# Kernel tuning notes

Hardware: AMD Instinct MI355X
Metric: run time of the kernel (lower is better)

The kernel has to match this reference:

```python
import jax, jax.numpy as jnp
import numpy as np
import math

D_MODEL = 512
NUM_HEADS = 8
B, L = 2, 4096
EPS_NORM = 1e-8
PLASTICITY = 1.0


def setup_inputs() -> dict:
    key = jax.random.key(0)
    ks = jax.random.split(key, 6)
    D, H = D_MODEL, NUM_HEADS
    std = 1.0 / math.sqrt(D)
    x = jax.random.normal(ks[0], (B, L, D), dtype=jnp.float32)
    qkv_w = jax.random.normal(ks[1], (3 * D, D), dtype=jnp.float32) * std
    qkv_b = jnp.zeros((3 * D,), dtype=jnp.float32)
    out_w = jax.random.normal(ks[2], (D, D), dtype=jnp.float32) * std
    out_b = jnp.zeros((D,), dtype=jnp.float32)
    decay_w = jax.random.normal(ks[3], (H, D), dtype=jnp.float32) * 0.02
    decay_b = jnp.full((H,), 4.0, dtype=jnp.float32)
    norm_scale = jnp.ones((D,), dtype=jnp.float32)
    return {"x": x, "qkv_w": qkv_w, "qkv_b": qkv_b, "out_w": out_w,
            "out_b": out_b, "decay_w": decay_w, "decay_b": decay_b,
            "norm_scale": norm_scale}


def _hebbian_forward(x, qkv_w, qkv_b, out_w, out_b, decay_w, decay_b, norm_scale):
    Bsz, Lsz, D = x.shape
    H = NUM_HEADS
    E = D // H
    # QKV projection (torch Linear: y = x @ W.T + b)
    qkv = x @ qkv_w.T + qkv_b
    q, k, v = jnp.split(qkv, 3, axis=-1)
    q = q.reshape(Bsz, Lsz, H, E)
    k = k.reshape(Bsz, Lsz, H, E)
    v = v.reshape(Bsz, Lsz, H, E)
    # feature map: elu(x) + 1
    q = (jax.nn.elu(q) + 1.0) / math.sqrt(E)
    k = jax.nn.elu(k) + 1.0
    # input-dependent decay per head
    decay_logits = x @ decay_w.T + decay_b          # (B,L,H)
    lambdas = (0.9 + 0.1 * jax.nn.sigmoid(decay_logits)) * PLASTICITY
    log_lambdas = jnp.log(jnp.clip(lambdas, 1e-6))[..., None]   # (B,L,H,1)
    log_lambda_cum = jnp.clip(jnp.cumsum(log_lambdas, axis=1), -50.0, 50.0)
    decay_k = jnp.exp(-log_lambda_cum)
    decay_q = jnp.exp(log_lambda_cum)
    k_decayed = k * decay_k
    q_decayed = q * decay_q
    # outer-product memory state cumsum: (B,L,H,E,E)
    kv = jnp.einsum('blhe,blhf->blhef', k_decayed, v)
    memory_state = jnp.cumsum(kv, axis=1)
    k_sum_decayed = jnp.cumsum(k_decayed, axis=1)
    num = jnp.einsum('blhe,blhef->blhf', q_decayed, memory_state)
    den = jnp.einsum('blhe,blhe->blh', q_decayed, k_sum_decayed)[..., None] + 1e-6
    out = (num / den).reshape(Bsz, Lsz, D)
    out = out @ out_w.T + out_b
    # RMSNorm (dropout is identity in eval)
    rnorm = jax.lax.rsqrt(jnp.mean(out * out, axis=-1, keepdims=True) + EPS_NORM)
    return out * rnorm * norm_scale


def reference(x, qkv_w, qkv_b, out_w, out_b, decay_w, decay_b, norm_scale):
    return _hebbian_forward(x, qkv_w, qkv_b, out_w, out_b, decay_w, decay_b, norm_scale)
```

## Files before the change

### kernel.cpp

```cpp
#include <hip/hip_runtime.h>

typedef unsigned short u16;
typedef unsigned int u32;

#define B_ 2
#define L_ 4096
#define D_ 512
#define H_ 8
#define E_ 64
#define M_ (B_*L_)
#define TD (3*D_)
#define NCH (L_/64)
#define BH (B_*H_)

typedef short bf16x8 __attribute__((ext_vector_type(8)));
typedef float f32x4 __attribute__((ext_vector_type(4)));

__device__ __forceinline__ float bf2f(u16 u){ return __uint_as_float(((u32)u)<<16); }
__device__ __forceinline__ u16 f2bf(float f){
  u32 u = __float_as_uint(f);
  u32 r = u + 0x7FFFu + ((u>>16)&1u);
  return (u16)(r>>16);
}
__device__ __forceinline__ float elu1(float v){ return v>0.f ? v+1.f : expf(v); }

__device__ __forceinline__ void async_ld16(const u16* g, u16* l){
  __builtin_amdgcn_global_load_lds(
      (const __attribute__((address_space(1))) void*)g,
      (__attribute__((address_space(3))) void*)l, 16, 0, 0);
}

__global__ __launch_bounds__(256) void decay_conv_kernel(const float* __restrict__ x,
    const float* __restrict__ dw, const float* __restrict__ db,
    const float* __restrict__ qw, const float* __restrict__ ow,
    float* __restrict__ ll, u16* __restrict__ xb,
    u16* __restrict__ qwb, u16* __restrict__ owb)
{
  int blk = blockIdx.x;
  if (blk < 2048){
    int wv = threadIdx.x>>6, lane = threadIdx.x&63;
    int m = blk*4 + wv;
    float xr[8];
    #pragma unroll
    for (int i=0;i<8;i++) xr[i] = x[(size_t)m*D_ + lane + 64*i];
    #pragma unroll
    for (int i=0;i<8;i++) xb[(size_t)m*D_ + lane + 64*i] = f2bf(xr[i]);
    int b = m >> 12, l = m & (L_-1);
    for (int h=0; h<H_; h++){
      float acc = 0.f;
      #pragma unroll
      for (int i=0;i<8;i++) acc += xr[i]*dw[h*D_ + lane + 64*i];
      #pragma unroll
      for (int off=32; off>0; off>>=1) acc += __shfl_xor(acc, off);
      if (lane == h){
        float z = acc + db[h];
        float lam = 0.9f + 0.1f/(1.f + expf(-z));
        ll[((b*H_+h)*L_) + l] = logf(lam);
      }
    }
  } else {
    int gid = (blk-2048)*256 + threadIdx.x;
    const float* src; u16* dst; int off;
    if (gid < 196608){ src = qw; dst = qwb; off = gid; }
    else { src = ow; dst = owb; off = gid - 196608; }
    float4 v = ((const float4*)src)[off];
    ushort4 o; o.x=f2bf(v.x); o.y=f2bf(v.y); o.z=f2bf(v.z); o.w=f2bf(v.w);
    ((ushort4*)dst)[off] = o;
  }
}

__global__ __launch_bounds__(256) void scan_kernel(const float* __restrict__ ll,
    float* __restrict__ cb)
{
  int bh = blockIdx.x, t = threadIdx.x;
  int lane = t & 63, wv = t >> 6;
  const float* p = ll + (size_t)bh*L_ + t*16;
  float s[16];
  #pragma unroll
  for (int q=0;q<4;q++){
    float4 v = *(const float4*)(p + q*4);
    s[q*4+0]=v.x; s[q*4+1]=v.y; s[q*4+2]=v.z; s[q*4+3]=v.w;
  }
  #pragma unroll
  for (int i=1;i<16;i++) s[i] += s[i-1];
  float tot = s[15];
  float ws = tot;
  #pragma unroll
  for (int off=1; off<64; off<<=1){
    float tmp = __shfl_up(ws, off);
    if (lane >= off) ws += tmp;
  }
  __shared__ float wsum[4];
  if (lane == 63) wsum[wv] = ws;
  __syncthreads();
  float base = 0.f;
  #pragma unroll
  for (int w2=0; w2<3; w2++) if (w2 < wv) base += wsum[w2];
  float ex = base + ws - tot;
  float* c = cb + (size_t)bh*L_ + t*16;
  #pragma unroll
  for (int i=0;i<16;i++) c[i] = fminf(50.f, fmaxf(-50.f, ex + s[i]));
}

template<bool OB>
__global__ __launch_bounds__(256) void gemm_mfma(const u16* __restrict__ A,
    const u16* __restrict__ W, const float* __restrict__ bias,
    void* __restrict__ Cv, int M, int N, int K)
{
  __shared__ u16 As[128*32];
  __shared__ u16 Bs[128*32];
  int n0 = blockIdx.x*128, m0 = blockIdx.y*128;
  int t = threadIdx.x, wave = t>>6, lane = t&63;
  int wm = (wave>>1)*64, wn = (wave&1)*64;
  f32x4 acc[4][4] = {};
  int srow = wave*32 + (lane>>2);
  int scol = (lane&3)*8;
  const u16* gA = A + (size_t)(m0+srow)*K + scol;
  const u16* gB = W + (size_t)(n0+srow)*K + scol;
  u16* lA = As + wave*1024;
  u16* lB = Bs + wave*1024;
  int q8 = (lane>>4)*8, r16 = lane&15;
  for (int k0=0; k0<K; k0+=32){
    async_ld16(gA + k0,                lA);
    async_ld16(gA + k0 + 16*(size_t)K, lA + 512);
    async_ld16(gB + k0,                lB);
    async_ld16(gB + k0 + 16*(size_t)K, lB + 512);
    __syncthreads();
    bf16x8 af[4], bfr[4];
    #pragma unroll
    for (int i=0;i<4;i++) af[i]  = *(const bf16x8*)&As[(wm + i*16 + r16)*32 + q8];
    #pragma unroll
    for (int j=0;j<4;j++) bfr[j] = *(const bf16x8*)&Bs[(wn + j*16 + r16)*32 + q8];
    #pragma unroll
    for (int i=0;i<4;i++)
      #pragma unroll
      for (int j=0;j<4;j++)
        acc[i][j] = __builtin_amdgcn_mfma_f32_16x16x32_bf16(af[i], bfr[j], acc[i][j], 0,0,0);
    __syncthreads();
  }
  #pragma unroll
  for (int i=0;i<4;i++){
    int row = m0 + wm + i*16 + (lane>>4)*4;
    #pragma unroll
    for (int j=0;j<4;j++){
      int col = n0 + wn + j*16 + r16;
      float bv = bias[col];
      #pragma unroll
      for (int r=0;r<4;r++){
        float val = acc[i][j][r] + bv;
        if (OB) ((u16*)Cv)[(size_t)(row+r)*N + col] = f2bf(val);
        else    ((float*)Cv)[(size_t)(row+r)*N + col] = val;
      }
    }
  }
}

__global__ __launch_bounds__(256) void transform_sums_kernel(const u16* __restrict__ qkvb,
    const float* __restrict__ cb, u16* __restrict__ qc, u16* __restrict__ kc,
    u16* __restrict__ vtc, u16* __restrict__ Stc, float* __restrict__ ksc)
{
  int bid = blockIdx.x;
  int bh = bid >> 6, ch = bid & 63;
  int b = bh >> 3, h = bh & 7;
  __shared__ u16 Ks[64*68];
  __shared__ u16 Vs[64*68];
  __shared__ u16 Ktl[4096];
  __shared__ u16 Vtl[4096];
  __shared__ float ksr[256];
  int t = threadIdx.x;
  size_t mbase = (size_t)b*L_ + ch*64;
  #pragma unroll
  for (int i=0;i<2;i++){
    int idx = t + 256*i;
    int l = idx>>3, e0 = (idx&7)*8;
    int kh = e0>>5, ej = e0&31;
    float c = cb[(size_t)bh*L_ + ch*64 + l];
    float eqc = expf(c)*0.125f, ekc = expf(-c);
    const u16* src = qkvb + (mbase+l)*TD + h*64 + e0;
    u16 in[8], o[8];
    *(ushort4*)&in[0] = *(const ushort4*)(src);
    *(ushort4*)&in[4] = *(const ushort4*)(src+4);
    #pragma unroll
    for (int j=0;j<8;j++) o[j] = f2bf(elu1(bf2f(in[j]))*eqc);
    u16* qd = qc + ((size_t)bid*2 + kh)*2048 + l*32 + ej;
    *(ushort4*)qd = *(ushort4*)&o[0];
    *(ushort4*)(qd+4) = *(ushort4*)&o[4];
    *(ushort4*)&in[0] = *(const ushort4*)(src + D_);
    *(ushort4*)&in[4] = *(const ushort4*)(src + D_ + 4);
    #pragma unroll
    for (int j=0;j<8;j++) o[j] = f2bf(elu1(bf2f(in[j]))*ekc);
    u16* kd = kc + ((size_t)bid*2 + kh)*2048 + l*32 + ej;
    *(ushort4*)kd = *(ushort4*)&o[0];
    *(ushort4*)(kd+4) = *(ushort4*)&o[4];
    *(ushort4*)&Ks[l*68+e0]   = *(ushort4*)&o[0];
    *(ushort4*)&Ks[l*68+e0+4] = *(ushort4*)&o[4];
    *(ushort4*)&Vs[l*68+e0]   = *(const ushort4*)(src + 2*D_);
    *(ushort4*)&Vs[l*68+e0+4] = *(const ushort4*)(src + 2*D_ + 4);
  }
  __syncthreads();
  int e = t & 63, jq = t >> 6;
  {
    u16 kv[16], vv[16];
    float ksum = 0.f;
    #pragma unroll
    for (int jj=0;jj<16;jj++){
      int j = jq*16+jj;
      kv[jj] = Ks[j*68 + e];
      ksum += bf2f(kv[jj]);
      vv[jj] = Vs[j*68 + e];
    }
    int kh = jq>>1, jl = (jq&1)*16;
    u16* kt = &Ktl[(kh*64 + e)*32 + jl];
    u16* vt = &Vtl[(kh*64 + e)*32 + jl];
    #pragma unroll
    for (int s=0;s<4;s++){
      *(ushort4*)(kt + s*4) = *(ushort4*)&kv[s*4];
      *(ushort4*)(vt + s*4) = *(ushort4*)&vv[s*4];
    }
    ksr[t] = ksum;
  }
  __syncthreads();
  {
    *(uint4*)&vtc[(size_t)bid*4096 + t*8]        = *(const uint4*)&Vtl[t*8];
    *(uint4*)&vtc[(size_t)bid*4096 + 2048 + t*8] = *(const uint4*)&Vtl[2048 + t*8];
  }
  int w = t>>6, lane = t&63;
  int r16 = lane & 15, q8 = (lane>>4)*8;
  bf16x8 av[2];
  #pragma unroll
  for (int kh=0;kh<2;kh++)
    av[kh] = *(const bf16x8*)&Vtl[(kh*64 + w*16 + r16)*32 + q8];
  f32x4 acc[4] = {};
  #pragma unroll
  for (int et=0;et<4;et++)
    #pragma unroll
    for (int kh=0;kh<2;kh++){
      bf16x8 bv = *(const bf16x8*)&Ktl[(kh*64 + et*16 + r16)*32 + q8];
      acc[et] = __builtin_amdgcn_mfma_f32_16x16x32_bf16(av[kh], bv, acc[et], 0,0,0);
    }
  #pragma unroll
  for (int et=0;et<4;et++){
    int eh = et>>1, el = (et&1)*16 + r16;
    #pragma unroll
    for (int r=0;r<4;r++){
      int f = w*16 + (lane>>4)*4 + r;
      Stc[((size_t)bid*2 + eh)*2048 + f*32 + el] = f2bf(acc[et][r]);
    }
  }
  if (t < 64) ksc[bid*64 + t] = ksr[t] + ksr[64+t] + ksr[128+t] + ksr[192+t];
}

__global__ __launch_bounds__(256) void chunk_prefix_kernel(u16* __restrict__ Stc,
    float* __restrict__ ksc)
{
  int gid = blockIdx.x*256 + threadIdx.x;
  int bh = gid >> 11, e2 = gid & 2047;
  u32* p = (u32*)Stc + (size_t)bh*131072 + e2;
  float r0 = 0.f, r1 = 0.f;
  #pragma unroll 4
  for (int ch=0; ch<NCH; ch++){
    u32 v = p[ch*2048];
    float lo = bf2f((u16)(v & 0xffffu));
    float hi = bf2f((u16)(v >> 16));
    p[ch*2048] = (u32)f2bf(r0) | ((u32)f2bf(r1) << 16);
    r0 += lo; r1 += hi;
  }
  if (gid < BH*64){
    int bh2 = gid >> 6, e = gid & 63;
    float* kp = ksc + bh2*4096 + e;
    float kr = 0.f;
    #pragma unroll 4
    for (int ch=0; ch<NCH; ch++){
      float v = kp[ch*64]; kp[ch*64] = kr; kr += v;
    }
  }
}

__global__ __launch_bounds__(256) void chunk_out_kernel(const u16* __restrict__ qc,
    const u16* __restrict__ kc, const u16* __restrict__ vtc,
    const u16* __restrict__ Stc, const float* __restrict__ ksc,
    u16* __restrict__ attn)
{
  int bid = blockIdx.x;
  int bh = bid >> 6, ch = bid & 63;
  int b = bh >> 3, h = bh & 7;
  __shared__ u16 KV[16384];
  __shared__ u16 Ab[4096];
  __shared__ float kp[64], den4[256], den[64];
  int t = threadIdx.x, w = t>>6, lane = t&63;
  size_t mbase = (size_t)b*L_ + ch*64;
  const u16* srcs[4] = { qc, kc, vtc, Stc };
  {
    const u16* gbase = srcs[w] + (size_t)bid*4096 + lane*8;
    #pragma unroll
    for (int q=0;q<8;q++)
      async_ld16(gbase + q*512, KV + w*4096 + q*512);
  }
  if (t < 64) kp[t] = ksc[bid*64 + t];
  __syncthreads();
  const u16* Qs   = KV;
  const u16* Kb_s = KV + 4096;
  const u16* Vt_s = KV + 8192;
  const u16* St_s = KV + 12288;
  int r16 = lane & 15, q8 = (lane>>4)*8;
  bf16x8 aq[2];
  #pragma unroll
  for (int eh=0;eh<2;eh++)
    aq[eh] = *(const bf16x8*)&Qs[(eh*64 + w*16 + r16)*32 + q8];
  f32x4 accA[4] = {};
  #pragma unroll
  for (int jt=0;jt<4;jt++)
    #pragma unroll
    for (int eh=0;eh<2;eh++){
      bf16x8 bv = *(const bf16x8*)&Kb_s[(eh*64 + jt*16 + r16)*32 + q8];
      accA[jt] = __builtin_amdgcn_mfma_f32_16x16x32_bf16(aq[eh], bv, accA[jt], 0,0,0);
    }
  int l4 = t>>2, q4 = t&3;
  float dkp = 0.f;
  {
    int eh = q4>>1, el0 = (q4&1)*16;
    bf16x8 x1 = *(const bf16x8*)&Qs[(eh*64 + l4)*32 + el0];
    bf16x8 x2 = *(const bf16x8*)&Qs[(eh*64 + l4)*32 + el0 + 8];
    #pragma unroll
    for (int i=0;i<8;i++)
      dkp += bf2f((u16)x1[i])*kp[q4*16+i] + bf2f((u16)x2[i])*kp[q4*16+8+i];
  }
  #pragma unroll
  for (int jt=0;jt<4;jt++)
    #pragma unroll
    for (int r=0;r<4;r++){
      int lr = w*16 + ((lane>>4)<<2) + r;
      int j  = jt*16 + r16;
      Ab[((jt>>1)*64 + lr)*32 + (jt&1)*16 + r16] = (j <= lr) ? f2bf(accA[jt][r]) : (u16)0;
    }
  __syncthreads();
  float dA = 0.f;
  {
    int jh2 = q4>>1, jl0 = (q4&1)*16;
    bf16x8 y1 = *(const bf16x8*)&Ab[(jh2*64 + l4)*32 + jl0];
    bf16x8 y2 = *(const bf16x8*)&Ab[(jh2*64 + l4)*32 + jl0 + 8];
    #pragma unroll
    for (int i=0;i<8;i++) dA += bf2f((u16)y1[i]) + bf2f((u16)y2[i]);
  }
  den4[t] = dkp + dA;
  __syncthreads();
  if (t < 64) den[t] = den4[t*4] + den4[t*4+1] + den4[t*4+2] + den4[t*4+3] + 1e-6f;
  bf16x8 aA[2];
  #pragma unroll
  for (int jh=0;jh<2;jh++)
    aA[jh] = *(const bf16x8*)&Ab[(jh*64 + w*16 + r16)*32 + q8];
  f32x4 acc[4] = {};
  #pragma unroll
  for (int ft=0;ft<4;ft++){
    #pragma unroll
    for (int jh=0;jh<2;jh++){
      bf16x8 bv = *(const bf16x8*)&Vt_s[(jh*64 + ft*16 + r16)*32 + q8];
      acc[ft] = __builtin_amdgcn_mfma_f32_16x16x32_bf16(aA[jh], bv, acc[ft], 0,0,0);
    }
    #pragma unroll
    for (int eh=0;eh<2;eh++){
      bf16x8 bv = *(const bf16x8*)&St_s[(eh*64 + ft*16 + r16)*32 + q8];
      acc[ft] = __builtin_amdgcn_mfma_f32_16x16x32_bf16(aq[eh], bv, acc[ft], 0,0,0);
    }
  }
  __syncthreads();
  float inv[4];
  #pragma unroll
  for (int r=0;r<4;r++) inv[r] = 1.f / den[w*16 + ((lane>>4)<<2) + r];
  #pragma unroll
  for (int ft=0;ft<4;ft++)
    #pragma unroll
    for (int r=0;r<4;r++){
      int lr = w*16 + ((lane>>4)<<2) + r;
      attn[(mbase + lr)*D_ + h*64 + ft*16 + r16] = f2bf(acc[ft][r]*inv[r]);
    }
}

__global__ __launch_bounds__(256) void rmsnorm_kernel(const u16* __restrict__ mid,
    const float* __restrict__ scale, float* __restrict__ out)
{
  int m = blockIdx.x, t = threadIdx.x;
  const u16* row = mid + (size_t)m*D_;
  float v0 = bf2f(row[t]), v1 = bf2f(row[t+256]);
  float ss = v0*v0 + v1*v1;
  #pragma unroll
  for (int off=32; off>0; off>>=1) ss += __shfl_xor(ss, off);
  __shared__ float red[4];
  if ((t&63)==0) red[t>>6] = ss;
  __syncthreads();
  float tot = red[0]+red[1]+red[2]+red[3];
  float r = rsqrtf(tot*(1.f/512.f) + 1e-8f);
  out[(size_t)m*D_ + t]       = v0*r*scale[t];
  out[(size_t)m*D_ + t + 256] = v1*r*scale[t+256];
}

extern "C" void kernel_launch(void* const* d_in, const int* in_sizes, int n_in,
                              void* d_out, int out_size, void* d_ws, size_t ws_size,
                              hipStream_t stream)
{
  const float* x     = (const float*)d_in[0];
  const float* w_qkv = (const float*)d_in[1];
  const float* b_qkv = (const float*)d_in[2];
  const float* w_out = (const float*)d_in[3];
  const float* b_out = (const float*)d_in[4];
  const float* w_dec = (const float*)d_in[5];
  const float* b_dec = (const float*)d_in[6];
  const float* gnorm = (const float*)d_in[7];
  float* out = (float*)d_out;

  char* ws = (char*)d_ws;
  u16*   qkvb = (u16*)(ws);
  u16*   qc   = (u16*)(ws + 25165824);
  u16*   kc   = (u16*)(ws + 33554432);
  u16*   vtc  = (u16*)(ws + 41943040);
  u16*   Stc  = (u16*)(ws + 50331648);
  float* ksc  = (float*)(ws + 58720256);
  float* ll   = (float*)(ws + 58982400);
  float* cb   = (float*)(ws + 59244544);
  u16*   xb   = (u16*)(ws + 59506688);
  u16*   qwb  = (u16*)(ws + 67895296);
  u16*   owb  = (u16*)(ws + 69468160);
  u16*   midb = qkvb;
  u16*   attn = xb;

  decay_conv_kernel<<<dim3(3072), dim3(256), 0, stream>>>(x, w_dec, b_dec, w_qkv, w_out,
                                                          ll, xb, qwb, owb);
  scan_kernel<<<dim3(BH), dim3(256), 0, stream>>>(ll, cb);
  gemm_mfma<true><<<dim3(TD/128, M_/128), dim3(256), 0, stream>>>(xb, qwb, b_qkv, qkvb, M_, TD, D_);
  transform_sums_kernel<<<dim3(BH*NCH), dim3(256), 0, stream>>>(qkvb, cb, qc, kc, vtc, Stc, ksc);
  chunk_prefix_kernel<<<dim3(128), dim3(256), 0, stream>>>(Stc, ksc);
  chunk_out_kernel<<<dim3(BH*NCH), dim3(256), 0, stream>>>(qc, kc, vtc, Stc, ksc, attn);
  gemm_mfma<true><<<dim3(D_/128, M_/128), dim3(256), 0, stream>>>(attn, owb, b_out, midb, M_, D_, D_);
  rmsnorm_kernel<<<dim3(M_), dim3(256), 0, stream>>>(midb, gnorm, out);
}
```

Before: 172.2 us.

## Fuse output projection with RMSNorm and pad LDS tiles in transform kernel

Replaces the output-projection GEMM plus separate RMSNorm with one kernel where each block computes a full 32x512 row slab and normalizes it in registers. This removes the bf16 intermediate round trip and one launch. It also pads the LDS tiles in transform_sums to cut bank conflicts, widens the loads and stores to 16 bytes, and switches to fast __expf. The key-sum prefix moves to its own blocks in chunk_prefix. The fused GEMM keeps the whole 512-column W tile in LDS with no double buffering and launches only 256 blocks, so occupancy and latency hiding may suffer.

After: 160.8 us. -6.6%, faster.

```diff
diff --git a/kernel.cpp b/kernel.cpp
--- a/kernel.cpp
+++ b/kernel.cpp
@@ -22,7 +22,7 @@
   u32 r = u + 0x7FFFu + ((u>>16)&1u);
   return (u16)(r>>16);
 }
-__device__ __forceinline__ float elu1(float v){ return v>0.f ? v+1.f : expf(v); }
+__device__ __forceinline__ float elu1(float v){ return v>0.f ? v+1.f : __expf(v); }
 
 __device__ __forceinline__ void async_ld16(const u16* g, u16* l){
   __builtin_amdgcn_global_load_lds(
@@ -54,7 +54,7 @@
       for (int off=32; off>0; off>>=1) acc += __shfl_xor(acc, off);
       if (lane == h){
         float z = acc + db[h];
-        float lam = 0.9f + 0.1f/(1.f + expf(-z));
+        float lam = 0.9f + 0.1f/(1.f + __expf(-z));
         ll[((b*H_+h)*L_) + l] = logf(lam);
       }
     }
@@ -162,10 +162,10 @@
   int bid = blockIdx.x;
   int bh = bid >> 6, ch = bid & 63;
   int b = bh >> 3, h = bh & 7;
-  __shared__ u16 Ks[64*68];
-  __shared__ u16 Vs[64*68];
-  __shared__ u16 Ktl[4096];
-  __shared__ u16 Vtl[4096];
+  __shared__ u16 Ks[64*72];
+  __shared__ u16 Vs[64*72];
+  __shared__ u16 Ktl[128*40];
+  __shared__ u16 Vtl[128*40];
   __shared__ float ksr[256];
   int t = threadIdx.x;
   size_t mbase = (size_t)b*L_ + ch*64;
@@ -175,67 +175,60 @@
     int l = idx>>3, e0 = (idx&7)*8;
     int kh = e0>>5, ej = e0&31;
     float c = cb[(size_t)bh*L_ + ch*64 + l];
-    float eqc = expf(c)*0.125f, ekc = expf(-c);
+    float eqc = __expf(c)*0.125f, ekc = __expf(-c);
     const u16* src = qkvb + (mbase+l)*TD + h*64 + e0;
-    u16 in[8], o[8];
-    *(ushort4*)&in[0] = *(const ushort4*)(src);
-    *(ushort4*)&in[4] = *(const ushort4*)(src+4);
-    #pragma unroll
-    for (int j=0;j<8;j++) o[j] = f2bf(elu1(bf2f(in[j]))*eqc);
-    u16* qd = qc + ((size_t)bid*2 + kh)*2048 + l*32 + ej;
-    *(ushort4*)qd = *(ushort4*)&o[0];
-    *(ushort4*)(qd+4) = *(ushort4*)&o[4];
-    *(ushort4*)&in[0] = *(const ushort4*)(src + D_);
-    *(ushort4*)&in[4] = *(const ushort4*)(src + D_ + 4);
-    #pragma unroll
-    for (int j=0;j<8;j++) o[j] = f2bf(elu1(bf2f(in[j]))*ekc);
-    u16* kd = kc + ((size_t)bid*2 + kh)*2048 + l*32 + ej;
-    *(ushort4*)kd = *(ushort4*)&o[0];
-    *(ushort4*)(kd+4) = *(ushort4*)&o[4];
-    *(ushort4*)&Ks[l*68+e0]   = *(ushort4*)&o[0];
-    *(ushort4*)&Ks[l*68+e0+4] = *(ushort4*)&o[4];
-    *(ushort4*)&Vs[l*68+e0]   = *(const ushort4*)(src + 2*D_);
-    *(ushort4*)&Vs[l*68+e0+4] = *(const ushort4*)(src + 2*D_ + 4);
+    union { uint4 v; u16 s[8]; } in, o;
+    in.v = *(const uint4*)src;
+    #pragma unroll
+    for (int j=0;j<8;j++) o.s[j] = f2bf(elu1(bf2f(in.s[j]))*eqc);
+    *(uint4*)(qc + ((size_t)bid*2 + kh)*2048 + l*32 + ej) = o.v;
+    in.v = *(const uint4*)(src + D_);
+    #pragma unroll
+    for (int j=0;j<8;j++) o.s[j] = f2bf(elu1(bf2f(in.s[j]))*ekc);
+    *(uint4*)(kc + ((size_t)bid*2 + kh)*2048 + l*32 + ej) = o.v;
+    *(uint4*)&Ks[l*72+e0] = o.v;
+    *(uint4*)&Vs[l*72+e0] = *(const uint4*)(src + 2*D_);
   }
   __syncthreads();
   int e = t & 63, jq = t >> 6;
   {
-    u16 kv[16], vv[16];
+    u16 kv[16] __attribute__((aligned(16)));
+    u16 vv[16] __attribute__((aligned(16)));
     float ksum = 0.f;
     #pragma unroll
     for (int jj=0;jj<16;jj++){
       int j = jq*16+jj;
-      kv[jj] = Ks[j*68 + e];
+      kv[jj] = Ks[j*72 + e];
       ksum += bf2f(kv[jj]);
-      vv[jj] = Vs[j*68 + e];
+      vv[jj] = Vs[j*72 + e];
     }
     int kh = jq>>1, jl = (jq&1)*16;
-    u16* kt = &Ktl[(kh*64 + e)*32 + jl];
-    u16* vt = &Vtl[(kh*64 + e)*32 + jl];
-    #pragma unroll
-    for (int s=0;s<4;s++){
-      *(ushort4*)(kt + s*4) = *(ushort4*)&kv[s*4];
-      *(ushort4*)(vt + s*4) = *(ushort4*)&vv[s*4];
-    }
+    u16* kt = &Ktl[(kh*64 + e)*40 + jl];
+    u16* vt = &Vtl[(kh*64 + e)*40 + jl];
+    *(uint4*)kt     = *(const uint4*)&kv[0];
+    *(uint4*)(kt+8) = *(const uint4*)&kv[8];
+    *(uint4*)vt     = *(const uint4*)&vv[0];
+    *(uint4*)(vt+8) = *(const uint4*)&vv[8];
     ksr[t] = ksum;
   }
   __syncthreads();
   {
-    *(uint4*)&vtc[(size_t)bid*4096 + t*8]        = *(const uint4*)&Vtl[t*8];
-    *(uint4*)&vtc[(size_t)bid*4096 + 2048 + t*8] = *(const uint4*)&Vtl[2048 + t*8];
+    int row = t>>1, c0 = (t&1)*16;
+    *(uint4*)&vtc[(size_t)bid*4096 + row*32 + c0]     = *(const uint4*)&Vtl[row*40 + c0];
+    *(uint4*)&vtc[(size_t)bid*4096 + row*32 + c0 + 8] = *(const uint4*)&Vtl[row*40 + c0 + 8];
   }
   int w = t>>6, lane = t&63;
   int r16 = lane & 15, q8 = (lane>>4)*8;
   bf16x8 av[2];
   #pragma unroll
   for (int kh=0;kh<2;kh++)
-    av[kh] = *(const bf16x8*)&Vtl[(kh*64 + w*16 + r16)*32 + q8];
+    av[kh] = *(const bf16x8*)&Vtl[(kh*64 + w*16 + r16)*40 + q8];
   f32x4 acc[4] = {};
   #pragma unroll
   for (int et=0;et<4;et++)
     #pragma unroll
     for (int kh=0;kh<2;kh++){
-      bf16x8 bv = *(const bf16x8*)&Ktl[(kh*64 + et*16 + r16)*32 + q8];
+      bf16x8 bv = *(const bf16x8*)&Ktl[(kh*64 + et*16 + r16)*40 + q8];
       acc[et] = __builtin_amdgcn_mfma_f32_16x16x32_bf16(av[kh], bv, acc[et], 0,0,0);
     }
   #pragma unroll
@@ -253,23 +246,26 @@
 __global__ __launch_bounds__(256) void chunk_prefix_kernel(u16* __restrict__ Stc,
     float* __restrict__ ksc)
 {
-  int gid = blockIdx.x*256 + threadIdx.x;
-  int bh = gid >> 11, e2 = gid & 2047;
-  u32* p = (u32*)Stc + (size_t)bh*131072 + e2;
-  float r0 = 0.f, r1 = 0.f;
-  #pragma unroll 4
-  for (int ch=0; ch<NCH; ch++){
-    u32 v = p[ch*2048];
-    float lo = bf2f((u16)(v & 0xffffu));
-    float hi = bf2f((u16)(v >> 16));
-    p[ch*2048] = (u32)f2bf(r0) | ((u32)f2bf(r1) << 16);
-    r0 += lo; r1 += hi;
-  }
-  if (gid < BH*64){
-    int bh2 = gid >> 6, e = gid & 63;
+  int blk = blockIdx.x, t = threadIdx.x;
+  if (blk < 128){
+    int gid = blk*256 + t;
+    int bh = gid >> 11, e2 = gid & 2047;
+    u32* p = (u32*)Stc + (size_t)bh*131072 + e2;
+    float r0 = 0.f, r1 = 0.f;
+    #pragma unroll 8
+    for (int ch=0; ch<NCH; ch++){
+      u32 v = p[ch*2048];
+      float lo = bf2f((u16)(v & 0xffffu));
+      float hi = bf2f((u16)(v >> 16));
+      p[ch*2048] = (u32)f2bf(r0) | ((u32)f2bf(r1) << 16);
+      r0 += lo; r1 += hi;
+    }
+  } else {
+    int gid2 = (blk-128)*256 + t;
+    int bh2 = gid2 >> 6, e = gid2 & 63;
     float* kp = ksc + bh2*4096 + e;
     float kr = 0.f;
-    #pragma unroll 4
+    #pragma unroll 8
     for (int ch=0; ch<NCH; ch++){
       float v = kp[ch*64]; kp[ch*64] = kr; kr += v;
     }
@@ -376,22 +372,84 @@
     }
 }
 
-__global__ __launch_bounds__(256) void rmsnorm_kernel(const u16* __restrict__ mid,
-    const float* __restrict__ scale, float* __restrict__ out)
-{
-  int m = blockIdx.x, t = threadIdx.x;
-  const u16* row = mid + (size_t)m*D_;
-  float v0 = bf2f(row[t]), v1 = bf2f(row[t+256]);
-  float ss = v0*v0 + v1*v1;
-  #pragma unroll
-  for (int off=32; off>0; off>>=1) ss += __shfl_xor(ss, off);
-  __shared__ float red[4];
-  if ((t&63)==0) red[t>>6] = ss;
-  __syncthreads();
-  float tot = red[0]+red[1]+red[2]+red[3];
-  float r = rsqrtf(tot*(1.f/512.f) + 1e-8f);
-  out[(size_t)m*D_ + t]       = v0*r*scale[t];
-  out[(size_t)m*D_ + t + 256] = v1*r*scale[t+256];
+__global__ __launch_bounds__(256) void gemm_rms_kernel(const u16* __restrict__ A,
+    const u16* __restrict__ W, const float* __restrict__ bias,
+    const float* __restrict__ gnorm, float* __restrict__ out)
+{
+  __shared__ u16 As[32*32];
+  __shared__ u16 Bs[512*32];
+  __shared__ float ssq_l[4][32];
+  __shared__ float rinv_l[32];
+  int m0 = blockIdx.x*32;
+  int t = threadIdx.x, wave = t>>6, lane = t&63;
+  int wn = wave*128;
+  int r16 = lane&15, q8 = (lane>>4)*8;
+  f32x4 acc[2][8] = {};
+  int scol = (t&3)*8;
+  const u16* gB = W + (size_t)(t>>2)*512 + scol;
+  const u16* gA = A + (size_t)(m0 + (t>>2))*512 + scol;
+  u16* lB = Bs + wave*512;
+  u16* lA = As + wave*512;
+  for (int k0=0; k0<512; k0+=32){
+    if (wave < 2) async_ld16(gA + k0, lA);
+    #pragma unroll
+    for (int it=0; it<8; it++)
+      async_ld16(gB + k0 + it*32768, lB + it*2048);
+    __syncthreads();
+    bf16x8 af[2];
+    af[0] = *(const bf16x8*)&As[r16*32 + q8];
+    af[1] = *(const bf16x8*)&As[(16 + r16)*32 + q8];
+    #pragma unroll
+    for (int j=0;j<8;j++){
+      bf16x8 bv = *(const bf16x8*)&Bs[(wn + j*16 + r16)*32 + q8];
+      acc[0][j] = __builtin_amdgcn_mfma_f32_16x16x32_bf16(af[0], bv, acc[0][j], 0,0,0);
+      acc[1][j] = __builtin_amdgcn_mfma_f32_16x16x32_bf16(af[1], bv, acc[1][j], 0,0,0);
+    }
+    __syncthreads();
+  }
+  int g = lane>>4;
+  float bv8[8], gv8[8];
+  #pragma unroll
+  for (int j=0;j<8;j++){ int col = wn + j*16 + r16; bv8[j] = bias[col]; gv8[j] = gnorm[col]; }
+  float ssq[2][4] = {};
+  #pragma unroll
+  for (int i=0;i<2;i++)
+    #pragma unroll
+    for (int j=0;j<8;j++)
+      #pragma unroll
+      for (int r=0;r<4;r++){
+        float v = acc[i][j][r] + bv8[j];
+        acc[i][j][r] = v;
+        ssq[i][r] += v*v;
+      }
+  #pragma unroll
+  for (int off=1; off<16; off<<=1)
+    #pragma unroll
+    for (int i=0;i<2;i++)
+      #pragma unroll
+      for (int r=0;r<4;r++)
+        ssq[i][r] += __shfl_xor(ssq[i][r], off);
+  if (r16 == 0){
+    #pragma unroll
+    for (int i=0;i<2;i++)
+      #pragma unroll
+      for (int r=0;r<4;r++)
+        ssq_l[wave][i*16 + g*4 + r] = ssq[i][r];
+  }
+  __syncthreads();
+  if (t < 32)
+    rinv_l[t] = rsqrtf((ssq_l[0][t]+ssq_l[1][t]+ssq_l[2][t]+ssq_l[3][t])*(1.f/512.f) + 1e-8f);
+  __syncthreads();
+  #pragma unroll
+  for (int i=0;i<2;i++)
+    #pragma unroll
+    for (int r=0;r<4;r++){
+      int row = m0 + i*16 + g*4 + r;
+      float ri = rinv_l[i*16 + g*4 + r];
+      #pragma unroll
+      for (int j=0;j<8;j++)
+        out[(size_t)row*512 + wn + j*16 + r16] = acc[i][j][r]*ri*gv8[j];
+    }
 }
 
 extern "C" void kernel_launch(void* const* d_in, const int* in_sizes, int n_in,
@@ -420,7 +478,6 @@
   u16*   xb   = (u16*)(ws + 59506688);
   u16*   qwb  = (u16*)(ws + 67895296);
   u16*   owb  = (u16*)(ws + 69468160);
-  u16*   midb = qkvb;
   u16*   attn = xb;
 
   decay_conv_kernel<<<dim3(3072), dim3(256), 0, stream>>>(x, w_dec, b_dec, w_qkv, w_out,
@@ -428,8 +485,7 @@
   scan_kernel<<<dim3(BH), dim3(256), 0, stream>>>(ll, cb);
   gemm_mfma<true><<<dim3(TD/128, M_/128), dim3(256), 0, stream>>>(xb, qwb, b_qkv, qkvb, M_, TD, D_);
   transform_sums_kernel<<<dim3(BH*NCH), dim3(256), 0, stream>>>(qkvb, cb, qc, kc, vtc, Stc, ksc);
-  chunk_prefix_kernel<<<dim3(128), dim3(256), 0, stream>>>(Stc, ksc);
+  chunk_prefix_kernel<<<dim3(132), dim3(256), 0, stream>>>(Stc, ksc);
   chunk_out_kernel<<<dim3(BH*NCH), dim3(256), 0, stream>>>(qc, kc, vtc, Stc, ksc, attn);
-  gemm_mfma<true><<<dim3(D_/128, M_/128), dim3(256), 0, stream>>>(attn, owb, b_out, midb, M_, D_, D_);
-  rmsnorm_kernel<<<dim3(M_), dim3(256), 0, stream>>>(midb, gnorm, out);
-}
+  gemm_rms_kernel<<<dim3(M_/32), dim3(256), 0, stream>>>(attn, owb, b_out, gnorm, out);
+}
```
